# Kernel tuning notes

Hardware: AMD Instinct MI355X
Metric: run time of the kernel (lower is better)

Reference implementation:

```python
import jax, jax.numpy as jnp
import numpy as np

EMB = 768
HEADS = 12
DK = EMB // HEADS


def setup_inputs() -> dict:
    key = jax.random.key(0)
    ks = jax.random.split(key, 11)
    B, S = 2, 2048
    lim = 1.0 / np.sqrt(EMB)
    def lin(k):
        kw, kb = jax.random.split(k)
        W = jax.random.uniform(kw, (EMB, EMB), jnp.float32, -lim, lim)
        b = jax.random.uniform(kb, (EMB,), jnp.float32, -lim, lim)
        return W, b
    Wq, bq = lin(ks[0])
    Wk, bk = lin(ks[1])
    Wv, bv = lin(ks[2])
    Wo, bo = lin(ks[3])
    return {
        "query": jax.random.normal(ks[4], (B, S, EMB), jnp.float32),
        "key": jax.random.normal(ks[5], (B, S, EMB), jnp.float32),
        "value": jax.random.normal(ks[6], (B, S, EMB), jnp.float32),
        "Wq": Wq, "bq": bq, "Wk": Wk, "bk": bk,
        "Wv": Wv, "bv": bv, "Wo": Wo, "bo": bo,
    }


def reference(query, key, value, Wq, bq, Wk, bk, Wv, bv, Wo, bo):
    B, S, _ = query.shape
    # nn.Linear: x @ W^T + b, then split heads -> [B, H, S, d_k]
    def proj(x, W, b):
        return (x @ W.T + b).reshape(B, -1, HEADS, DK).transpose(0, 2, 1, 3)
    q = proj(query, Wq, bq)
    k = proj(key, Wk, bk)
    v = proj(value, Wv, bv)
    scale = 1.0 / jnp.sqrt(jnp.float32(DK))
    scores = jnp.einsum('bhqd,bhkd->bhqk', q, k) * scale  # [B,H,S,S]
    attn = jax.nn.softmax(scores, axis=-1)
    av = jnp.einsum('bhqk,bhkd->bhqd', attn, v)
    concat = av.transpose(0, 2, 1, 3).reshape(B, -1, EMB)
    return concat @ Wo.T + bo
```

## Files before the change

### kernel.cpp

```cpp
#include <hip/hip_runtime.h>
#include <hip/hip_bf16.h>

#define EMB 768
#define HEADS 12
#define DKV 64
#define BATCH 2
#define SEQ 2048
#define NTOK (BATCH*SEQ)

typedef float f32x4 __attribute__((ext_vector_type(4)));
typedef unsigned short u16;
typedef u16 u16x8 __attribute__((ext_vector_type(8)));
typedef u16 u16x4 __attribute__((ext_vector_type(4)));
typedef __bf16 bf16x8 __attribute__((ext_vector_type(8)));

__device__ __forceinline__ u16 f2bf(float f) {
  return __builtin_bit_cast(u16, (__bf16)f);
}
__device__ __forceinline__ float fexp2(float x) {
#if __has_builtin(__builtin_amdgcn_exp2f)
  return __builtin_amdgcn_exp2f(x);
#else
  return exp2f(x);
#endif
}
__device__ __forceinline__ f32x4 mfma16(u16x8 a, u16x8 b, f32x4 c) {
  return __builtin_amdgcn_mfma_f32_16x16x32_bf16(
      __builtin_bit_cast(bf16x8, a), __builtin_bit_cast(bf16x8, b), c, 0, 0, 0);
}

template<int MODE, bool AF32>
__device__ __forceinline__ void gemm_core(
    const void* __restrict__ Ap, const float* __restrict__ Bm,
    const float* __restrict__ bias, float ascale, float bscale,
    void* __restrict__ outp, u16* __restrict__ At, u16* __restrict__ Bt,
    int m0, int n0)
{
  const int t = threadIdx.x;
  const int w = t >> 6, lane = t & 63, lg = lane >> 4, lr = lane & 15;
  const int wr = w >> 1, wc = w & 1;
  const int tr = t >> 3, tsl = t & 7;

  f32x4 acc[2][2] = {};
  f32x4 raf[2][2];
  u16x8 rab[2];
  f32x4 rbf[2][2];

  auto STAGE_LOAD = [&](int kb) {
    #pragma unroll
    for (int q = 0; q < 2; ++q) {
      int row = q*32 + tr;
      if constexpr (AF32) {
        const float* p = (const float*)Ap + (size_t)(m0+row)*EMB + kb + tsl*8;
        raf[q][0] = *reinterpret_cast<const f32x4*>(p);
        raf[q][1] = *reinterpret_cast<const f32x4*>(p + 4);
      } else {
        rab[q] = *reinterpret_cast<const u16x8*>(
            (const u16*)Ap + (size_t)(m0+row)*EMB + kb + tsl*8);
      }
    }
    #pragma unroll
    for (int q = 0; q < 2; ++q) {
      int row = q*32 + tr;
      const float* p = Bm + (size_t)(n0+row)*EMB + kb + tsl*8;
      rbf[q][0] = *reinterpret_cast<const f32x4*>(p);
      rbf[q][1] = *reinterpret_cast<const f32x4*>(p + 4);
    }
  };

  auto STAGE_WRITE = [&](int bi) {
    #pragma unroll
    for (int q = 0; q < 2; ++q) {
      int row = q*32 + tr;
      u16x8 v;
      if constexpr (AF32) {
        #pragma unroll
        for (int j = 0; j < 4; ++j) {
          v[j]   = f2bf(raf[q][0][j] * ascale);
          v[4+j] = f2bf(raf[q][1][j] * ascale);
        }
      } else v = rab[q];
      *reinterpret_cast<u16x8*>(&At[bi*4096 + row*64 + ((tsl ^ (row & 7))*8)]) = v;
    }
    #pragma unroll
    for (int q = 0; q < 2; ++q) {
      int row = q*32 + tr;
      u16x8 v;
      #pragma unroll
      for (int j = 0; j < 4; ++j) {
        v[j]   = f2bf(rbf[q][0][j]);
        v[4+j] = f2bf(rbf[q][1][j]);
      }
      *reinterpret_cast<u16x8*>(&Bt[bi*4096 + row*64 + ((tsl ^ (row & 7))*8)]) = v;
    }
  };

  auto COMPUTE = [&](int bi) {
    u16x8 af[2][2], bfr[2][2];
    #pragma unroll
    for (int fm = 0; fm < 2; ++fm)
      #pragma unroll
      for (int kk = 0; kk < 2; ++kk) {
        int r = wr*32 + fm*16 + lr;
        int slot = (lg + 4*kk) ^ (r & 7);
        af[fm][kk] = *reinterpret_cast<const u16x8*>(&At[bi*4096 + r*64 + slot*8]);
      }
    #pragma unroll
    for (int fn = 0; fn < 2; ++fn)
      #pragma unroll
      for (int kk = 0; kk < 2; ++kk) {
        int r = wc*32 + fn*16 + lr;
        int slot = (lg + 4*kk) ^ (r & 7);
        bfr[fn][kk] = *reinterpret_cast<const u16x8*>(&Bt[bi*4096 + r*64 + slot*8]);
      }
    __builtin_amdgcn_s_setprio(1);
    #pragma unroll
    for (int fm = 0; fm < 2; ++fm)
      #pragma unroll
      for (int fn = 0; fn < 2; ++fn)
        #pragma unroll
        for (int kk = 0; kk < 2; ++kk)
          acc[fm][fn] = mfma16(af[fm][kk], bfr[fn][kk], acc[fm][fn]);
    __builtin_amdgcn_s_setprio(0);
  };

  STAGE_LOAD(0);
  STAGE_WRITE(0);
  __syncthreads();
  const int NSTEP = EMB/64;
  #pragma unroll
  for (int ts = 0; ts < NSTEP-1; ++ts) {
    STAGE_LOAD((ts+1)*64);
    COMPUTE(ts & 1);
    STAGE_WRITE((ts & 1) ^ 1);
    __syncthreads();
  }
  COMPUTE((NSTEP-1) & 1);

  #pragma unroll
  for (int fm = 0; fm < 2; ++fm)
    #pragma unroll
    for (int fn = 0; fn < 2; ++fn) {
      const int mb = m0 + wr*32 + fm*16 + lg*4;
      const int e  = n0 + wc*32 + fn*16 + lr;
      if constexpr (MODE == 2) {
        int bb = mb >> 11, sb = mb & 2047, h = e >> 6, d = e & 63;
        u16x4 o4;
        #pragma unroll
        for (int j = 0; j < 4; ++j) o4[j] = f2bf(acc[fm][fn][j] + bias[e]*bscale);
        *reinterpret_cast<u16x4*>(
            reinterpret_cast<u16*>(outp) + (((size_t)(bb*HEADS+h))*DKV + d)*SEQ + sb) = o4;
      } else {
        #pragma unroll
        for (int j = 0; j < 4; ++j) {
          int m = mb + j;
          float val = acc[fm][fn][j] + bias[e]*bscale;
          if constexpr (MODE == 0) {
            int bb = m >> 11, s = m & 2047, h = e >> 6, d = e & 63;
            reinterpret_cast<u16*>(outp)[(((size_t)(bb*HEADS+h))*SEQ + s)*DKV + d] = f2bf(val);
          } else {
            reinterpret_cast<float*>(outp)[(size_t)m*EMB + e] = val;
          }
        }
      }
    }
}

__global__ __launch_bounds__(256) void qkv_k(
    const float* __restrict__ Aq, const float* __restrict__ Ak, const float* __restrict__ Av,
    const float* __restrict__ Wq, const float* __restrict__ Wk, const float* __restrict__ Wv,
    const float* __restrict__ bq, const float* __restrict__ bk, const float* __restrict__ bv,
    u16* __restrict__ Qh, u16* __restrict__ Kh, u16* __restrict__ Vh, float csc)
{
  __shared__ __align__(16) u16 At[2*64*64];
  __shared__ __align__(16) u16 Bt[2*64*64];
  const int m0 = blockIdx.x*64, n0 = blockIdx.y*64;
  const int z = blockIdx.z;
  if (z == 0)
    gemm_core<0,true>(Aq, Wq, bq, csc, csc, Qh, At, Bt, m0, n0);
  else if (z == 1)
    gemm_core<0,true>(Ak, Wk, bk, 1.f, 1.f, Kh, At, Bt, m0, n0);
  else
    gemm_core<2,true>(Av, Wv, bv, 1.f, 1.f, Vh, At, Bt, m0, n0);
}

__global__ __launch_bounds__(256) void gemm_out_k(
    const u16* __restrict__ A, const float* __restrict__ Bm,
    const float* __restrict__ bias, float* __restrict__ outp)
{
  __shared__ __align__(16) u16 At[2*64*64];
  __shared__ __align__(16) u16 Bt[2*64*64];
  gemm_core<1,false>(A, Bm, bias, 1.f, 1.f, outp, At, Bt, blockIdx.x*64, blockIdx.y*64);
}

__global__ __launch_bounds__(256) void flash_attn_k(
    const u16* __restrict__ Q, const u16* __restrict__ K, const u16* __restrict__ VT,
    u16* __restrict__ av)
{
  __shared__ __align__(16) u16 Kt[2][64*64];
  __shared__ __align__(16) u16 Vt[2][64*64];
  __shared__ __align__(16) u16 Pt[4][2][16*64];

  const int t = threadIdx.x;
  const int w = t >> 6, lane = t & 63, lg = lane >> 4, lr = lane & 15;
  const int tr = t >> 3, tsl = t & 7;
  const int qb = blockIdx.x;
  const int bh = blockIdx.y;
  const u16* Qb = Q  + (size_t)bh*SEQ*DKV;
  const u16* Kb = K  + (size_t)bh*SEQ*DKV;
  const u16* Vb = VT + (size_t)bh*DKV*SEQ;

  const int qrow = qb*64 + w*16 + lr;
  u16x8 qf[2];
  qf[0] = *reinterpret_cast<const u16x8*>(Qb + (size_t)qrow*DKV + lg*8);
  qf[1] = *reinterpret_cast<const u16x8*>(Qb + (size_t)qrow*DKV + 32 + lg*8);

  f32x4 acc[4] = {};
  float mrun = -1e30f, lrun = 0.f;
  f32x4 s[4];

  u16x8 ks[2], vs[2];
  auto LOADKV = [&](int kt0) {
    #pragma unroll
    for (int q = 0; q < 2; ++q) {
      int row = q*32 + tr;
      ks[q] = *reinterpret_cast<const u16x8*>(Kb + (size_t)(kt0+row)*DKV + tsl*8);
    }
    #pragma unroll
    for (int q = 0; q < 2; ++q) {
      int d = q*32 + tr;
      vs[q] = *reinterpret_cast<const u16x8*>(Vb + (size_t)d*SEQ + kt0 + tsl*8);
    }
  };

  const int NT = SEQ/64;

#define WKV(bi)                                                               \
  do {                                                                        \
    _Pragma("unroll")                                                         \
    for (int q = 0; q < 2; ++q) {                                             \
      int row = q*32 + tr;                                                    \
      *reinterpret_cast<u16x8*>(&Kt[bi][row*64 + ((tsl ^ (row & 7))*8)]) = ks[q]; \
    }                                                                         \
    _Pragma("unroll")                                                         \
    for (int q = 0; q < 2; ++q) {                                             \
      int d = q*32 + tr;                                                      \
      *reinterpret_cast<u16x8*>(&Vt[bi][d*64 + ((tsl ^ (d & 7))*8)]) = vs[q]; \
    }                                                                         \
  } while (0)

#define QK_MFMA(bi)                                                           \
  do {                                                                        \
    _Pragma("unroll")                                                         \
    for (int fc = 0; fc < 4; ++fc) {                                          \
      f32x4 z = {};                                                           \
      _Pragma("unroll")                                                       \
      for (int kk = 0; kk < 2; ++kk) {                                        \
        int r = fc*16 + lr;                                                   \
        int slot = (lg + 4*kk) ^ (r & 7);                                     \
        u16x8 kf = *reinterpret_cast<const u16x8*>(&Kt[bi][r*64 + slot*8]);   \
        z = mfma16(kf, qf[kk], z);                                            \
      }                                                                       \
      s[fc] = z;                                                              \
    }                                                                         \
  } while (0)

#define PV_MFMA(bi)                                                           \
  do {                                                                        \
    const char* Pr = reinterpret_cast<const char*>(&Pt[w][bi][0]);            \
    _Pragma("unroll")                                                         \
    for (int kk = 0; kk < 2; ++kk) {                                          \
      u16x8 pf = *reinterpret_cast<const u16x8*>(                             \
          Pr + lr*128 + (((kk*8 + lg*2) ^ ((lr & 7) << 1))*8));               \
      _Pragma("unroll")                                                       \
      for (int fc = 0; fc < 4; ++fc) {                                        \
        int rv = fc*16 + lr;                                                  \
        int slotv = (lg + 4*kk) ^ (rv & 7);                                   \
        u16x8 vf = *reinterpret_cast<const u16x8*>(&Vt[bi][rv*64 + slotv*8]); \
        acc[fc] = mfma16(vf, pf, acc[fc]);                                    \
      }                                                                       \
    }                                                                         \
  } while (0)

#define SOFTMAX_PW(bi)                                                        \
  do {                                                                        \
    float a0 = fmaxf(fmaxf(s[0][0], s[0][1]), s[0][2]);                       \
    float a1 = fmaxf(fmaxf(s[0][3], s[1][0]), s[1][1]);                       \
    float a2 = fmaxf(fmaxf(s[1][2], s[1][3]), s[2][0]);                       \
    float a3 = fmaxf(fmaxf(s[2][1], s[2][2]), s[2][3]);                       \
    float a4 = fmaxf(fmaxf(s[3][0], s[3][1]), s[3][2]);                       \
    float pmax = fmaxf(fmaxf(fmaxf(a0, a1), a2),                              \
                       fmaxf(fmaxf(a3, a4), s[3][3]));                        \
    if (__any(pmax > mrun + 8.f)) {          \
      float pm = fmaxf(pmax, __shfl_xor(pmax, 16));                           \
      pm = fmaxf(pm, __shfl_xor(pm, 32));                                     \
      float mnew = fmaxf(mrun, pm);                                           \
      float corr = fexp2(mrun - mnew);                                        \
      mrun = mnew; lrun *= corr;                                              \
      _Pragma("unroll")                                                       \
      for (int fc = 0; fc < 4; ++fc)                                          \
        _Pragma("unroll")                                                     \
        for (int j = 0; j < 4; ++j)                                           \
          acc[fc][j] *= corr;                                                 \
    }                                                                         \
    float p[4][4], rsv[4];                                                    \
    _Pragma("unroll")                                                         \
    for (int fc = 0; fc < 4; ++fc) {                                          \
      _Pragma("unroll")                                                       \
      for (int j = 0; j < 4; ++j) p[fc][j] = fexp2(s[fc][j] - mrun);          \
      rsv[fc] = (p[fc][0] + p[fc][1]) + (p[fc][2] + p[fc][3]);                \
    }                                                                         \
    lrun += (rsv[0] + rsv[1]) + (rsv[2] + rsv[3]);                            \
    char* Pw_ = reinterpret_cast<char*>(&Pt[w][bi][0]);                       \
    _Pragma("unroll")                                                         \
    for (int fc = 0; fc < 4; ++fc) {                                          \
      u16x4 q4;                                                               \
      _Pragma("unroll")                                                       \
      for (int j = 0; j < 4; ++j) q4[j] = f2bf(p[fc][j]);                     \
      *reinterpret_cast<u16x4*>(                                              \
          Pw_ + lr*128 + (((fc*4 + lg) ^ ((lr & 7) << 1))*8)) = q4;           \
    }                                                                         \
  } while (0)

#define ITER(bi, kt)                                                          \
  do {                                                                        \
    __builtin_amdgcn_s_setprio(1);                                            \
    QK_MFMA(bi);                                                              \
    PV_MFMA(bi^1);                                                            \
    __builtin_amdgcn_s_setprio(0);                                            \
    SOFTMAX_PW(bi);                                                           \
    __syncthreads();                       \
    if ((kt)+1 < NT) WKV(bi^1);                  \
    __syncthreads();                                    \
    if ((kt)+2 < NT) LOADKV(((kt)+2)*64);                                     \
  } while (0)

  LOADKV(0);
  WKV(0);
  __syncthreads();
  LOADKV(64);
  QK_MFMA(0);
  SOFTMAX_PW(0);
  WKV(1);
  __syncthreads();
  LOADKV(128);

  for (int kt = 1; kt+1 < NT; kt += 2) {
    ITER(1, kt);
    ITER(0, kt+1);
  }
  ITER(1, NT-1);

  PV_MFMA(1);
  float lt = lrun;
  lt += __shfl_xor(lt, 16);
  lt += __shfl_xor(lt, 32);
  const float inv = 1.0f / lt;

  const int b = bh / HEADS, h = bh % HEADS;
  #pragma unroll
  for (int fc = 0; fc < 4; ++fc) {
    u16x4 o4;
    #pragma unroll
    for (int j = 0; j < 4; ++j) o4[j] = f2bf(acc[fc][j] * inv);
    *reinterpret_cast<u16x4*>(
        av + ((size_t)(b*SEQ + qrow))*EMB + h*64 + fc*16 + lg*4) = o4;
  }
#undef ITER
#undef SOFTMAX_PW
#undef PV_MFMA
#undef QK_MFMA
#undef WKV
}

extern "C" void kernel_launch(void* const* d_in, const int* in_sizes, int n_in,
                              void* d_out, int out_size, void* d_ws, size_t ws_size,
                              hipStream_t stream) {
  const float* xq_f = (const float*)d_in[0];
  const float* xk_f = (const float*)d_in[1];
  const float* xv_f = (const float*)d_in[2];
  const float* Wq = (const float*)d_in[3];
  const float* bq = (const float*)d_in[4];
  const float* Wk = (const float*)d_in[5];
  const float* bk = (const float*)d_in[6];
  const float* Wv = (const float*)d_in[7];
  const float* bv = (const float*)d_in[8];
  const float* Wo = (const float*)d_in[9];
  const float* bo = (const float*)d_in[10];

  u16* Qh = (u16*)d_ws;
  u16* Kh = Qh + (size_t)NTOK*EMB;
  u16* Vh = Kh + (size_t)NTOK*EMB;
  u16* Xb = Vh + (size_t)NTOK*EMB;

  const float csc = 0.125f * 1.4426950408889634f;

  qkv_k<<<dim3(NTOK/64, EMB/64, 3), dim3(256), 0, stream>>>(
      xq_f, xk_f, xv_f, Wq, Wk, Wv, bq, bk, bv, Qh, Kh, Vh, csc);

  flash_attn_k<<<dim3(SEQ/64, BATCH*HEADS), dim3(256), 0, stream>>>(Qh, Kh, Vh, Xb);

  gemm_out_k<<<dim3(NTOK/64, EMB/64), dim3(256), 0, stream>>>(Xb, Wo, bo, (float*)d_out);
}
```

Before: 101.3 us.

## Pre-cast inputs and weights to bf16, use 128x128 GEMM tiles with direct-to-LDS loads

```diff
diff --git a/kernel.cpp b/kernel.cpp
--- a/kernel.cpp
+++ b/kernel.cpp
@@ -28,121 +28,114 @@
   return __builtin_amdgcn_mfma_f32_16x16x32_bf16(
       __builtin_bit_cast(bf16x8, a), __builtin_bit_cast(bf16x8, b), c, 0, 0, 0);
 }
-
-template<int MODE, bool AF32>
+__device__ __forceinline__ void gload16(const void* g, void* l) {
+  __builtin_amdgcn_global_load_lds(
+      (const __attribute__((address_space(1))) void*)g,
+      (__attribute__((address_space(3))) void*)l, 16, 0, 0);
+}
+
+__global__ void cast_all_k(
+    const float* __restrict__ x0, const float* __restrict__ x1, const float* __restrict__ x2,
+    const float* __restrict__ w0, const float* __restrict__ w1,
+    const float* __restrict__ w2, const float* __restrict__ w3,
+    u16* __restrict__ X0, u16* __restrict__ X1, u16* __restrict__ X2,
+    u16* __restrict__ W0, u16* __restrict__ W1, u16* __restrict__ W2, u16* __restrict__ W3,
+    float wscale0)
+{
+  const int NX = NTOK*EMB/8;
+  const int NW = EMB*EMB/8;
+  const int total = 3*NX + 4*NW;
+  int i = blockIdx.x*256 + threadIdx.x;
+  for (; i < total; i += gridDim.x*256) {
+    const float* s; u16* d; int off; float sc = 1.f;
+    if (i < 3*NX) {
+      int which = i / NX; off = i - which*NX;
+      s = which==0 ? x0 : which==1 ? x1 : x2;
+      d = which==0 ? X0 : which==1 ? X1 : X2;
+    } else {
+      int j = i - 3*NX; int which = j / NW; off = j - which*NW;
+      s = which==0 ? w0 : which==1 ? w1 : which==2 ? w2 : w3;
+      d = which==0 ? W0 : which==1 ? W1 : which==2 ? W2 : W3;
+      if (which == 0) sc = wscale0;
+    }
+    float4 a = reinterpret_cast<const float4*>(s)[off*2];
+    float4 b = reinterpret_cast<const float4*>(s)[off*2+1];
+    u16x8 o;
+    o[0]=f2bf(a.x*sc); o[1]=f2bf(a.y*sc); o[2]=f2bf(a.z*sc); o[3]=f2bf(a.w*sc);
+    o[4]=f2bf(b.x*sc); o[5]=f2bf(b.y*sc); o[6]=f2bf(b.z*sc); o[7]=f2bf(b.w*sc);
+    reinterpret_cast<u16x8*>(d)[off] = o;
+  }
+}
+
+template<int MODE>
 __device__ __forceinline__ void gemm_core(
-    const void* __restrict__ Ap, const float* __restrict__ Bm,
-    const float* __restrict__ bias, float ascale, float bscale,
-    void* __restrict__ outp, u16* __restrict__ At, u16* __restrict__ Bt,
-    int m0, int n0)
+    const u16* __restrict__ A, const u16* __restrict__ Bm,
+    const float* __restrict__ bias, float bscale, void* __restrict__ outp,
+    u16* __restrict__ At, u16* __restrict__ Bt, int m0, int n0)
 {
   const int t = threadIdx.x;
   const int w = t >> 6, lane = t & 63, lg = lane >> 4, lr = lane & 15;
   const int wr = w >> 1, wc = w & 1;
-  const int tr = t >> 3, tsl = t & 7;
-
-  f32x4 acc[2][2] = {};
-  f32x4 raf[2][2];
-  u16x8 rab[2];
-  f32x4 rbf[2][2];
-
-  auto STAGE_LOAD = [&](int kb) {
-    #pragma unroll
-    for (int q = 0; q < 2; ++q) {
-      int row = q*32 + tr;
-      if constexpr (AF32) {
-        const float* p = (const float*)Ap + (size_t)(m0+row)*EMB + kb + tsl*8;
-        raf[q][0] = *reinterpret_cast<const f32x4*>(p);
-        raf[q][1] = *reinterpret_cast<const f32x4*>(p + 4);
-      } else {
-        rab[q] = *reinterpret_cast<const u16x8*>(
-            (const u16*)Ap + (size_t)(m0+row)*EMB + kb + tsl*8);
-      }
-    }
-    #pragma unroll
-    for (int q = 0; q < 2; ++q) {
-      int row = q*32 + tr;
-      const float* p = Bm + (size_t)(n0+row)*EMB + kb + tsl*8;
-      rbf[q][0] = *reinterpret_cast<const f32x4*>(p);
-      rbf[q][1] = *reinterpret_cast<const f32x4*>(p + 4);
+
+  f32x4 acc[4][4] = {};
+
+  const int crow = (w*4)*8 + (lane >> 3);
+  const int csl  = lane & 7;
+
+  auto STAGE = [&](int kb) {
+    #pragma unroll
+    for (int i = 0; i < 4; ++i) {
+      int row = crow + i*8;
+      int sg = csl ^ (row & 7);
+      gload16(A  + (size_t)(m0+row)*EMB + kb + sg*8, &At[(w*4+i)*512]);
+      gload16(Bm + (size_t)(n0+row)*EMB + kb + sg*8, &Bt[(w*4+i)*512]);
     }
   };
 
-  auto STAGE_WRITE = [&](int bi) {
-    #pragma unroll
-    for (int q = 0; q < 2; ++q) {
-      int row = q*32 + tr;
-      u16x8 v;
-      if constexpr (AF32) {
-        #pragma unroll
-        for (int j = 0; j < 4; ++j) {
-          v[j]   = f2bf(raf[q][0][j] * ascale);
-          v[4+j] = f2bf(raf[q][1][j] * ascale);
-        }
-      } else v = rab[q];
-      *reinterpret_cast<u16x8*>(&At[bi*4096 + row*64 + ((tsl ^ (row & 7))*8)]) = v;
-    }
-    #pragma unroll
-    for (int q = 0; q < 2; ++q) {
-      int row = q*32 + tr;
-      u16x8 v;
-      #pragma unroll
-      for (int j = 0; j < 4; ++j) {
-        v[j]   = f2bf(rbf[q][0][j]);
-        v[4+j] = f2bf(rbf[q][1][j]);
-      }
-      *reinterpret_cast<u16x8*>(&Bt[bi*4096 + row*64 + ((tsl ^ (row & 7))*8)]) = v;
-    }
-  };
-
-  auto COMPUTE = [&](int bi) {
-    u16x8 af[2][2], bfr[2][2];
-    #pragma unroll
-    for (int fm = 0; fm < 2; ++fm)
+  auto COMPUTE = [&]() {
+    u16x8 af[4][2], bf[4][2];
+    #pragma unroll
+    for (int fm = 0; fm < 4; ++fm)
       #pragma unroll
       for (int kk = 0; kk < 2; ++kk) {
-        int r = wr*32 + fm*16 + lr;
-        int slot = (lg + 4*kk) ^ (r & 7);
-        af[fm][kk] = *reinterpret_cast<const u16x8*>(&At[bi*4096 + r*64 + slot*8]);
+        int r = wr*64 + fm*16 + lr;
+        int p = (lg + 4*kk) ^ (r & 7);
+        af[fm][kk] = *reinterpret_cast<const u16x8*>(&At[r*64 + p*8]);
       }
     #pragma unroll
-    for (int fn = 0; fn < 2; ++fn)
+    for (int fn = 0; fn < 4; ++fn)
       #pragma unroll
       for (int kk = 0; kk < 2; ++kk) {
-        int r = wc*32 + fn*16 + lr;
-        int slot = (lg + 4*kk) ^ (r & 7);
-        bfr[fn][kk] = *reinterpret_cast<const u16x8*>(&Bt[bi*4096 + r*64 + slot*8]);
+        int r = wc*64 + fn*16 + lr;
+        int p = (lg + 4*kk) ^ (r & 7);
+        bf[fn][kk] = *reinterpret_cast<const u16x8*>(&Bt[r*64 + p*8]);
       }
     __builtin_amdgcn_s_setprio(1);
     #pragma unroll
-    for (int fm = 0; fm < 2; ++fm)
+    for (int fm = 0; fm < 4; ++fm)
       #pragma unroll
-      for (int fn = 0; fn < 2; ++fn)
+      for (int fn = 0; fn < 4; ++fn)
         #pragma unroll
         for (int kk = 0; kk < 2; ++kk)
-          acc[fm][fn] = mfma16(af[fm][kk], bfr[fn][kk], acc[fm][fn]);
+          acc[fm][fn] = mfma16(af[fm][kk], bf[fn][kk], acc[fm][fn]);
     __builtin_amdgcn_s_setprio(0);
   };
 
-  STAGE_LOAD(0);
-  STAGE_WRITE(0);
-  __syncthreads();
   const int NSTEP = EMB/64;
   #pragma unroll
-  for (int ts = 0; ts < NSTEP-1; ++ts) {
-    STAGE_LOAD((ts+1)*64);
-    COMPUTE(ts & 1);
-    STAGE_WRITE((ts & 1) ^ 1);
+  for (int ts = 0; ts < NSTEP; ++ts) {
+    STAGE(ts*64);
     __syncthreads();
+    COMPUTE();
+    if (ts+1 < NSTEP) __syncthreads();
   }
-  COMPUTE((NSTEP-1) & 1);
 
   #pragma unroll
-  for (int fm = 0; fm < 2; ++fm)
-    #pragma unroll
-    for (int fn = 0; fn < 2; ++fn) {
-      const int mb = m0 + wr*32 + fm*16 + lg*4;
-      const int e  = n0 + wc*32 + fn*16 + lr;
+  for (int fm = 0; fm < 4; ++fm)
+    #pragma unroll
+    for (int fn = 0; fn < 4; ++fn) {
+      const int mb = m0 + wr*64 + fm*16 + lg*4;
+      const int e  = n0 + wc*64 + fn*16 + lr;
       if constexpr (MODE == 2) {
         int bb = mb >> 11, sb = mb & 2047, h = e >> 6, d = e & 63;
         u16x4 o4;
@@ -167,30 +160,30 @@
 }
 
 __global__ __launch_bounds__(256) void qkv_k(
-    const float* __restrict__ Aq, const float* __restrict__ Ak, const float* __restrict__ Av,
-    const float* __restrict__ Wq, const float* __restrict__ Wk, const float* __restrict__ Wv,
+    const u16* __restrict__ Xq, const u16* __restrict__ Xk, const u16* __restrict__ Xv,
+    const u16* __restrict__ Wq, const u16* __restrict__ Wk, const u16* __restrict__ Wv,
     const float* __restrict__ bq, const float* __restrict__ bk, const float* __restrict__ bv,
     u16* __restrict__ Qh, u16* __restrict__ Kh, u16* __restrict__ Vh, float csc)
 {
-  __shared__ __align__(16) u16 At[2*64*64];
-  __shared__ __align__(16) u16 Bt[2*64*64];
-  const int m0 = blockIdx.x*64, n0 = blockIdx.y*64;
+  __shared__ __align__(16) u16 At[128*64];
+  __shared__ __align__(16) u16 Bt[128*64];
+  const int m0 = blockIdx.x*128, n0 = blockIdx.y*128;
   const int z = blockIdx.z;
   if (z == 0)
-    gemm_core<0,true>(Aq, Wq, bq, csc, csc, Qh, At, Bt, m0, n0);
+    gemm_core<0>(Xq, Wq, bq, csc, Qh, At, Bt, m0, n0);
   else if (z == 1)
-    gemm_core<0,true>(Ak, Wk, bk, 1.f, 1.f, Kh, At, Bt, m0, n0);
+    gemm_core<0>(Xk, Wk, bk, 1.f, Kh, At, Bt, m0, n0);
   else
-    gemm_core<2,true>(Av, Wv, bv, 1.f, 1.f, Vh, At, Bt, m0, n0);
+    gemm_core<2>(Xv, Wv, bv, 1.f, Vh, At, Bt, m0, n0);
 }
 
 __global__ __launch_bounds__(256) void gemm_out_k(
-    const u16* __restrict__ A, const float* __restrict__ Bm,
+    const u16* __restrict__ A, const u16* __restrict__ Bm,
     const float* __restrict__ bias, float* __restrict__ outp)
 {
-  __shared__ __align__(16) u16 At[2*64*64];
-  __shared__ __align__(16) u16 Bt[2*64*64];
-  gemm_core<1,false>(A, Bm, bias, 1.f, 1.f, outp, At, Bt, blockIdx.x*64, blockIdx.y*64);
+  __shared__ __align__(16) u16 At[128*64];
+  __shared__ __align__(16) u16 Bt[128*64];
+  gemm_core<1>(A, Bm, bias, 1.f, outp, At, Bt, blockIdx.x*128, blockIdx.y*128);
 }
 
 __global__ __launch_bounds__(256) void flash_attn_k(
@@ -388,17 +381,30 @@
   const float* Wo = (const float*)d_in[9];
   const float* bo = (const float*)d_in[10];
 
-  u16* Qh = (u16*)d_ws;
-  u16* Kh = Qh + (size_t)NTOK*EMB;
-  u16* Vh = Kh + (size_t)NTOK*EMB;
-  u16* Xb = Vh + (size_t)NTOK*EMB;
+  const size_t NX = (size_t)NTOK*EMB;
+  const size_t NW = (size_t)EMB*EMB;
+  u16* Xc0 = (u16*)d_ws;
+  u16* Xc1 = Xc0 + NX;
+  u16* Xc2 = Xc1 + NX;
+  u16* Wc0 = Xc2 + NX;
+  u16* Wc1 = Wc0 + NW;
+  u16* Wc2 = Wc1 + NW;
+  u16* Wc3 = Wc2 + NW;
+  u16* Qh  = Wc3 + NW;
+  u16* Kh  = Qh + NX;
+  u16* Vh  = Kh + NX;
+  u16* Xb  = Xc0;
 
   const float csc = 0.125f * 1.4426950408889634f;
 
-  qkv_k<<<dim3(NTOK/64, EMB/64, 3), dim3(256), 0, stream>>>(
-      xq_f, xk_f, xv_f, Wq, Wk, Wv, bq, bk, bv, Qh, Kh, Vh, csc);
+  cast_all_k<<<dim3(2048), dim3(256), 0, stream>>>(
+      xq_f, xk_f, xv_f, Wq, Wk, Wv, Wo,
+      Xc0, Xc1, Xc2, Wc0, Wc1, Wc2, Wc3, csc);
+
+  qkv_k<<<dim3(NTOK/128, EMB/128, 3), dim3(256), 0, stream>>>(
+      Xc0, Xc1, Xc2, Wc0, Wc1, Wc2, bq, bk, bv, Qh, Kh, Vh, csc);
 
   flash_attn_k<<<dim3(SEQ/64, BATCH*HEADS), dim3(256), 0, stream>>>(Qh, Kh, Vh, Xb);
 
-  gemm_out_k<<<dim3(NTOK/64, EMB/64), dim3(256), 0, stream>>>(Xb, Wo, bo, (float*)d_out);
-}
+  gemm_out_k<<<dim3(NTOK/128, EMB/128), dim3(256), 0, stream>>>(Xb, Wc3, bo, (float*)d_out);
+}
```

After: 104.8 us. +3.5%, slower.
